# Optimization experiments

Measured on AMD Instinct MI355X. Metric: run time of the kernel, lower is better.

## Reference

```python
import jax, jax.numpy as jnp
import numpy as np
from jax import lax

EPS = 1e-5

def _layernorm(x, g, b):
    m = x.mean(-1, keepdims=True)
    v = ((x - m) ** 2).mean(-1, keepdims=True)
    return (x - m) * lax.rsqrt(v + EPS) * g + b

def _batchnorm(x, g, b):
    # x: [N, C, L]; training-mode batch statistics (torch BatchNorm1d default)
    m = x.mean((0, 2), keepdims=True)
    v = ((x - m) ** 2).mean((0, 2), keepdims=True)
    return (x - m) * lax.rsqrt(v + EPS) * g[None, :, None] + b[None, :, None]

def _conv1d(x, w, bias, stride):
    y = lax.conv_general_dilated(x, w, window_strides=(stride,), padding='VALID',
                                 dimension_numbers=('NCH', 'OIH', 'NCH'))
    return y + bias[None, :, None]

def setup_inputs() -> dict:
    key = jax.random.key(0)
    ks = jax.random.split(key, 22)
    B, C, L = 512, 12, 5000
    NF, HID, LAT = 32, 64, 32
    def w(k, shape, fan_in):
        return jax.random.normal(k, shape, jnp.float32) * (1.0 / np.sqrt(fan_in))
    return {
        'x': jax.random.normal(ks[0], (B, C, L), jnp.float32),
        'c1w': w(ks[1], (32, C, 50), C * 50), 'c1b': jnp.zeros((32,), jnp.float32),
        'bn1g': jnp.ones((32,), jnp.float32), 'bn1b': jnp.zeros((32,), jnp.float32),
        'c2w': w(ks[2], (NF, 32, 25), 32 * 25), 'c2b': jnp.zeros((NF,), jnp.float32),
        'bn2g': jnp.ones((NF,), jnp.float32), 'bn2b': jnp.zeros((NF,), jnp.float32),
        'Wi': w(ks[3], (LAT, NF), NF) * 0.5, 'bi': jnp.zeros((LAT,), jnp.float32),
        'ln1g': jnp.ones((LAT,), jnp.float32), 'ln1b': jnp.zeros((LAT,), jnp.float32),
        'Wh': w(ks[4], (HID, LAT), LAT) * 0.5, 'bh': jnp.zeros((HID,), jnp.float32),
        'ln2g': jnp.ones((HID,), jnp.float32), 'ln2b': jnp.zeros((HID,), jnp.float32),
        'Wr': w(ks[5], (LAT, HID), HID) * 0.5, 'br': jnp.zeros((LAT,), jnp.float32),
        'Wo': w(ks[6], (LAT, LAT), LAT), 'bo': jnp.zeros((LAT,), jnp.float32),
    }

def reference(x, c1w, c1b, bn1g, bn1b, c2w, c2b, bn2g, bn2b,
              Wi, bi, ln1g, ln1b, Wh, bh, ln2g, ln2b, Wr, br, Wo, bo):
    # CNN front-end: [B,12,5000] -> [B,32,496] -> [B,32,95]
    h = jax.nn.relu(_batchnorm(_conv1d(x, c1w, c1b, 10), bn1g, bn1b))
    h = jax.nn.relu(_batchnorm(_conv1d(h, c2w, c2b, 5), bn2g, bn2b))
    feats = h.transpose(2, 0, 1)  # [T, B, NF]
    # input_proj + ln1 have no dependence on the recurrent state -> hoist out of loop
    xt_all = _layernorm(jnp.einsum('tbf,lf->tbl', feats, Wi) + bi, ln1g, ln1b)  # [T,B,LAT]

    def step(hstate, xt):
        combined = xt + hstate
        hp = jax.nn.relu(combined @ Wh.T + bh)      # [B, HID]
        hp = _layernorm(hp, ln2g, ln2b)
        hnew = jnp.tanh(hp @ Wr.T + br)             # [B, LAT]
        return hnew, hnew

    h0 = jnp.zeros((x.shape[0], Wr.shape[0]), x.dtype)
    _, outs = lax.scan(step, h0, xt_all)            # outs: [T, B, LAT]
    pooled = outs.mean(0)                           # mean over time
    return pooled @ Wo.T + bo                       # [B, LAT]
```

## Files before the change

kernel.cpp:

```cpp
#include <hip/hip_runtime.h>

#define EPS 1e-5f

#define B    512
#define C_IN 12
#define L_IN 5000
#define C1   32
#define L1   496
#define NF   32
#define L2   95
#define LAT  32
#define HID  64
#define T    L2

typedef short s16x8 __attribute__((ext_vector_type(8)));
typedef float f32x16 __attribute__((ext_vector_type(16)));

__device__ __forceinline__ ushort f2bf(float f) {
    uint u = __builtin_bit_cast(uint, f);
    u += 0x7fff + ((u >> 16) & 1);
    return (ushort)(u >> 16);
}
__device__ __forceinline__ float bf2f(ushort h) {
    return __builtin_bit_cast(float, (uint)h << 16);
}
__device__ __forceinline__ uint pk(float f) {
    ushort h = f2bf(f);
    return (uint)h | ((uint)f2bf(f - bf2f(h)) << 16);
}
__device__ __forceinline__ uint4 pack4(float4 d) {
    return make_uint4(pk(d.x), pk(d.y), pk(d.z), pk(d.w));
}

__global__ void k_prep_w(const float* __restrict__ c1w, const float* __restrict__ c2w,
                         ushort* __restrict__ wfrag1, ushort* __restrict__ wfrag2) {
    int i = blockIdx.x * 256 + threadIdx.x;
    if (i < 6144) {
        int lane = i & 63, r = i >> 6;
        int split = r & 1, s = (r >> 1) & 3, c = r >> 3;
        int oc = lane & 31, kbase = s * 16 + (lane >> 5) * 8;
        ushort o8[8];
#pragma unroll
        for (int j = 0; j < 8; ++j) {
            int kk = kbase + j;
            float w = (kk < 50) ? c1w[oc * 600 + c * 50 + kk] : 0.f;
            ushort hb = f2bf(w);
            o8[j] = split ? f2bf(w - bf2f(hb)) : hb;
        }
        ushort4* dst = reinterpret_cast<ushort4*>(wfrag1) + (size_t)i * 2;
        dst[0] = make_ushort4(o8[0], o8[1], o8[2], o8[3]);
        dst[1] = make_ushort4(o8[4], o8[5], o8[6], o8[7]);
    } else if (i < 14336) {
        int j = i - 6144;
        int lane = j & 63, r = j >> 6;
        int split = r & 1, ks = (r >> 1) & 1, c = r >> 2;
        int oc = lane & 31, kbase = ks * 16 + (lane >> 5) * 8;
        ushort o8[8];
#pragma unroll
        for (int jj = 0; jj < 8; ++jj) {
            int kk = kbase + jj;
            float w = (kk < 25) ? c2w[oc * 800 + c * 25 + kk] : 0.f;
            ushort hb = f2bf(w);
            o8[jj] = split ? f2bf(w - bf2f(hb)) : hb;
        }
        ushort4* dst = reinterpret_cast<ushort4*>(wfrag2) + (size_t)j * 2;
        dst[0] = make_ushort4(o8[0], o8[1], o8[2], o8[3]);
        dst[1] = make_ushort4(o8[4], o8[5], o8[6], o8[7]);
    }
}

__device__ __forceinline__ void conv1_compute(const uint (*xs)[1344], const uint4* wf4,
                                              int c0, int abase, int lane,
                                              f32x16& hh, f32x16& hl, f32x16& lh) {
    for (int cc = 0; cc < 6; ++cc) {
        const int c = c0 + cc;
        const uint* xc = xs[c];
        const uint4* wfc = wf4 + (size_t)c * 512 + lane;
#pragma unroll
        for (int s = 0; s < 4; ++s) {
            const int idx = abase + s * 16;
            uint2 p0 = *reinterpret_cast<const uint2*>(&xc[idx]);
            uint2 p1 = *reinterpret_cast<const uint2*>(&xc[idx + 2]);
            uint2 p2 = *reinterpret_cast<const uint2*>(&xc[idx + 4]);
            uint2 p3 = *reinterpret_cast<const uint2*>(&xc[idx + 6]);
            union { s16x8 v; uint u[4]; } ah, al, bh, bl;
            ah.u[0] = __builtin_amdgcn_perm(p0.y, p0.x, 0x05040100u);
            al.u[0] = __builtin_amdgcn_perm(p0.y, p0.x, 0x07060302u);
            ah.u[1] = __builtin_amdgcn_perm(p1.y, p1.x, 0x05040100u);
            al.u[1] = __builtin_amdgcn_perm(p1.y, p1.x, 0x07060302u);
            ah.u[2] = __builtin_amdgcn_perm(p2.y, p2.x, 0x05040100u);
            al.u[2] = __builtin_amdgcn_perm(p2.y, p2.x, 0x07060302u);
            ah.u[3] = __builtin_amdgcn_perm(p3.y, p3.x, 0x05040100u);
            al.u[3] = __builtin_amdgcn_perm(p3.y, p3.x, 0x07060302u);
            uint4 bq = wfc[s * 128];
            uint4 lq = wfc[s * 128 + 64];
            bh.u[0] = bq.x; bh.u[1] = bq.y; bh.u[2] = bq.z; bh.u[3] = bq.w;
            bl.u[0] = lq.x; bl.u[1] = lq.y; bl.u[2] = lq.z; bl.u[3] = lq.w;
            hh = __builtin_amdgcn_mfma_f32_32x32x16_bf16(ah.v, bh.v, hh, 0, 0, 0);
            hl = __builtin_amdgcn_mfma_f32_32x32x16_bf16(ah.v, bl.v, hl, 0, 0, 0);
            lh = __builtin_amdgcn_mfma_f32_32x32x16_bf16(al.v, bh.v, lh, 0, 0, 0);
        }
    }
}

__global__ __launch_bounds__(512, 4) void k_conv1(const float* __restrict__ x,
                                                  const ushort* __restrict__ wfrag,
                                                  const float* __restrict__ c1b,
                                                  float* __restrict__ y1,
                                                  float* __restrict__ raw1) {
    __shared__ uint xs[C_IN][1344];
    __shared__ float redS[4][32], redQ[4][32];
    const int chunk = blockIdx.x, b = blockIdx.y, tid = threadIdx.x;
    const int t0 = chunk * 128;
    const int v4max = min(336, (5000 - 10 * t0) >> 2);
    const float4* xb4 = reinterpret_cast<const float4*>(x + (size_t)b * (C_IN * L_IN) + 10 * t0);

    uint4* xs4 = reinterpret_cast<uint4*>(&xs[0][0]);
#pragma unroll
    for (int r = 0; r < 2; ++r) {
        float4 rg[4];
#pragma unroll
        for (int i = 0; i < 4; ++i) {
            const int v = tid + (r * 4 + i) * 512;
            const int c = v / 336, i4 = v - c * 336;
            rg[i] = make_float4(0, 0, 0, 0);
            if (v < 4032 && i4 < v4max) rg[i] = xb4[c * 1250 + i4];
        }
#pragma unroll
        for (int i = 0; i < 4; ++i) {
            const int v = tid + (r * 4 + i) * 512;
            if (v < 4032) xs4[v] = pack4(rg[i]);
        }
    }
    __syncthreads();

    const int lane = tid & 63, wv = tid >> 6;
    const int g = wv >> 2;
    const int tw = wv & 3;
    const int cl = lane & 31;
    const int kgrp = lane >> 5;
    const int abase = 10 * (tw * 32 + cl) + kgrp * 8;

    f32x16 hh, hl, lh;
#pragma unroll
    for (int i = 0; i < 16; ++i) { hh[i] = 0.f; hl[i] = 0.f; lh[i] = 0.f; }
    const uint4* wf4 = reinterpret_cast<const uint4*>(wfrag);

    conv1_compute(xs, wf4, g * 6, abase, lane, hh, hl, lh);

    f32x16 tot;
#pragma unroll
    for (int i = 0; i < 16; ++i) tot[i] = hh[i] + hl[i] + lh[i];

    __syncthreads();
    float4* pr = reinterpret_cast<float4*>(&xs[0][0]);
    if (g == 1) {
#pragma unroll
        for (int i4 = 0; i4 < 4; ++i4)
            pr[tw * 256 + i4 * 64 + lane] =
                make_float4(tot[4*i4], tot[4*i4+1], tot[4*i4+2], tot[4*i4+3]);
    }
    __syncthreads();

    float sum = 0.f, sq = 0.f;
    if (g == 0) {
        const float bias = c1b[cl];
        float* yb = y1 + ((size_t)b * C1 + cl) * L1;
#pragma unroll
        for (int q = 0; q < 4; ++q) {
            float4 p = pr[tw * 256 + q * 64 + lane];
            const int trow = t0 + tw * 32 + 8 * q + 4 * kgrp;
            float4 st;
            st.x = tot[4*q+0] + p.x + bias;
            st.y = tot[4*q+1] + p.y + bias;
            st.z = tot[4*q+2] + p.z + bias;
            st.w = tot[4*q+3] + p.w + bias;
            if (trow < L1) {
                *reinterpret_cast<float4*>(yb + trow) = st;
                sum += st.x + st.y + st.z + st.w;
                sq  += st.x * st.x + st.y * st.y + st.z * st.z + st.w * st.w;
            }
        }
        sum += __shfl_xor(sum, 32);
        sq  += __shfl_xor(sq, 32);
        if (lane < 32) { redS[tw][cl] = sum; redQ[tw][cl] = sq; }
    }
    __syncthreads();
    if (tid < 64) {
        int o = tid & 31, isQ = tid >> 5;
        float v = isQ ? (redQ[0][o] + redQ[1][o] + redQ[2][o] + redQ[3][o])
                      : (redS[0][o] + redS[1][o] + redS[2][o] + redS[3][o]);
        atomicAdd(&raw1[(isQ ? 1024 : 0) + o * 16], v);
    }
}

__global__ __launch_bounds__(384, 3) void k_conv2(const float* __restrict__ y1,
                                                  const ushort* __restrict__ wfrag2,
                                                  const float* __restrict__ c2b,
                                                  const float* __restrict__ raw1,
                                                  const float* __restrict__ bn1g,
                                                  const float* __restrict__ bn1b,
                                                  float* __restrict__ y2,
                                                  float* __restrict__ raw2) {
    __shared__ uint xs[C1][512];
    __shared__ float fin[64];
    __shared__ float redS[3][32], redQ[3][32];
    const int b = blockIdx.x, tid = threadIdx.x;

    if (tid < 32) {
        const float cnt = 1.f / (float)(B * L1);
        float mean = raw1[tid * 16] * cnt;
        float var = raw1[1024 + tid * 16] * cnt - mean * mean;
        float sc = bn1g[tid] * rsqrtf(var + EPS);
        fin[tid] = sc;
        fin[32 + tid] = bn1b[tid] - mean * sc;
    }
    __syncthreads();

    const float4* src = reinterpret_cast<const float4*>(y1 + (size_t)b * (C1 * L1));
    for (int v = tid; v < C1 * 128; v += 384) {
        const int c = v >> 7, i4 = v & 127;
        uint4 o = make_uint4(0, 0, 0, 0);
        if (i4 < 124) {
            const float sc = fin[c], sh = fin[32 + c];
            float4 d = src[c * 124 + i4];
            float e0 = fmaxf(fmaf(d.x, sc, sh), 0.f);
            float e1 = fmaxf(fmaf(d.y, sc, sh), 0.f);
            float e2 = fmaxf(fmaf(d.z, sc, sh), 0.f);
            float e3 = fmaxf(fmaf(d.w, sc, sh), 0.f);
            o = make_uint4(pk(e0), pk(e1), pk(e2), pk(e3));
        }
        *reinterpret_cast<uint4*>(&xs[c][4 * i4]) = o;
    }
    __syncthreads();

    const int lane = tid & 63, wv = tid >> 6;
    const int g = (wv >= 3) ? 1 : 0;
    const int tw = wv - 3 * g;
    const int cl = lane & 31;
    const int kgrp = lane >> 5;
    const int tbase = 5 * (tw * 32 + cl) + kgrp * 8;

    f32x16 hh, hl, lh;
#pragma unroll
    for (int i = 0; i < 16; ++i) { hh[i] = 0.f; hl[i] = 0.f; lh[i] = 0.f; }
    const uint4* wf4 = reinterpret_cast<const uint4*>(wfrag2);

    for (int cc = 0; cc < 16; ++cc) {
        const int c = g * 16 + cc;
        const uint* xc = xs[c];
        const uint4* wfc = wf4 + (size_t)c * 256 + lane;
#pragma unroll
        for (int ks = 0; ks < 2; ++ks) {
            const int idx = tbase + ks * 16;
            uint u0 = xc[idx + 0], u1 = xc[idx + 1], u2 = xc[idx + 2], u3 = xc[idx + 3];
            uint u4 = xc[idx + 4], u5 = xc[idx + 5], u6 = xc[idx + 6], u7 = xc[idx + 7];
            union { s16x8 v; uint u[4]; } ah, al, bh, bl;
            ah.u[0] = __builtin_amdgcn_perm(u1, u0, 0x05040100u);
            al.u[0] = __builtin_amdgcn_perm(u1, u0, 0x07060302u);
            ah.u[1] = __builtin_amdgcn_perm(u3, u2, 0x05040100u);
            al.u[1] = __builtin_amdgcn_perm(u3, u2, 0x07060302u);
            ah.u[2] = __builtin_amdgcn_perm(u5, u4, 0x05040100u);
            al.u[2] = __builtin_amdgcn_perm(u5, u4, 0x07060302u);
            ah.u[3] = __builtin_amdgcn_perm(u7, u6, 0x05040100u);
            al.u[3] = __builtin_amdgcn_perm(u7, u6, 0x07060302u);
            uint4 bq = wfc[ks * 128];
            uint4 lq = wfc[ks * 128 + 64];
            bh.u[0] = bq.x; bh.u[1] = bq.y; bh.u[2] = bq.z; bh.u[3] = bq.w;
            bl.u[0] = lq.x; bl.u[1] = lq.y; bl.u[2] = lq.z; bl.u[3] = lq.w;
            hh = __builtin_amdgcn_mfma_f32_32x32x16_bf16(ah.v, bh.v, hh, 0, 0, 0);
            hl = __builtin_amdgcn_mfma_f32_32x32x16_bf16(ah.v, bl.v, hl, 0, 0, 0);
            lh = __builtin_amdgcn_mfma_f32_32x32x16_bf16(al.v, bh.v, lh, 0, 0, 0);
        }
    }

    f32x16 tot;
#pragma unroll
    for (int i = 0; i < 16; ++i) tot[i] = hh[i] + hl[i] + lh[i];

    __syncthreads();
    float4* pr = reinterpret_cast<float4*>(&xs[0][0]);
    if (g == 1) {
#pragma unroll
        for (int i4 = 0; i4 < 4; ++i4)
            pr[tw * 256 + i4 * 64 + lane] =
                make_float4(tot[4*i4], tot[4*i4+1], tot[4*i4+2], tot[4*i4+3]);
    }
    __syncthreads();

    float sum = 0.f, sq = 0.f;
    if (g == 0) {
        const float bias = c2b[cl];
#pragma unroll
        for (int q = 0; q < 4; ++q) {
            float4 p = pr[tw * 256 + q * 64 + lane];
            float v4[4] = { tot[4*q+0] + p.x + bias, tot[4*q+1] + p.y + bias,
                            tot[4*q+2] + p.z + bias, tot[4*q+3] + p.w + bias };
#pragma unroll
            for (int j = 0; j < 4; ++j) {
                const int t = tw * 32 + 8 * q + 4 * kgrp + j;
                if (t < L2) {
                    y2[((size_t)b * L2 + t) * NF + cl] = v4[j];
                    sum += v4[j]; sq += v4[j] * v4[j];
                }
            }
        }
        sum += __shfl_xor(sum, 32);
        sq  += __shfl_xor(sq, 32);
        if (lane < 32) { redS[tw][cl] = sum; redQ[tw][cl] = sq; }
    }
    __syncthreads();
    if (tid < 64) {
        int o = tid & 31, isQ = tid >> 5;
        float v = isQ ? (redQ[0][o] + redQ[1][o] + redQ[2][o])
                      : (redS[0][o] + redS[1][o] + redS[2][o]);
        atomicAdd(&raw2[(isQ ? 1024 : 0) + o * 16], v);
    }
}

__global__ __launch_bounds__(256) void k_proj(const float* __restrict__ y2,
                                              const float* __restrict__ raw2,
                                              const float* __restrict__ bn2g,
                                              const float* __restrict__ bn2b,
                                              const float* __restrict__ Wi,
                                              const float* __restrict__ bi,
                                              const float* __restrict__ ln1g,
                                              const float* __restrict__ ln1b,
                                              const float* __restrict__ Wh,
                                              const float* __restrict__ bh,
                                              float* __restrict__ xt2) {
    __shared__ float fin[64];
    if (threadIdx.x < 32) {
        const float cnt = 1.f / (float)(B * L2);
        float mean = raw2[threadIdx.x * 16] * cnt;
        float var = raw2[1024 + threadIdx.x * 16] * cnt - mean * mean;
        float sc = bn2g[threadIdx.x] * rsqrtf(var + EPS);
        fin[threadIdx.x] = sc;
        fin[32 + threadIdx.x] = bn2b[threadIdx.x] - mean * sc;
    }
    __syncthreads();

    const int r = blockIdx.x * 256 + threadIdx.x;
    const int b = r / 95, t = r - b * 95;

    const float4* row = reinterpret_cast<const float4*>(y2 + (size_t)r * NF);
    float u[NF];
#pragma unroll
    for (int f4 = 0; f4 < 8; ++f4) {
        float4 v = row[f4];
        u[4*f4]   = fmaxf(fmaf(v.x, fin[4*f4],   fin[32 + 4*f4]),   0.f);
        u[4*f4+1] = fmaxf(fmaf(v.y, fin[4*f4+1], fin[32 + 4*f4+1]), 0.f);
        u[4*f4+2] = fmaxf(fmaf(v.z, fin[4*f4+2], fin[32 + 4*f4+2]), 0.f);
        u[4*f4+3] = fmaxf(fmaf(v.w, fin[4*f4+3], fin[32 + 4*f4+3]), 0.f);
    }
    float xln[LAT];
    float s = 0.f, q = 0.f;
#pragma unroll
    for (int l = 0; l < LAT; ++l) {
        float a = bi[l];
#pragma unroll
        for (int f = 0; f < NF; ++f) a = fmaf(u[f], Wi[l * NF + f], a);
        xln[l] = a; s += a; q += a * a;
    }
    const float m = s * (1.f / LAT);
    const float inv = rsqrtf(q * (1.f / LAT) - m * m + EPS);
#pragma unroll
    for (int l = 0; l < LAT; ++l) xln[l] = (xln[l] - m) * inv * ln1g[l] + ln1b[l];

    float4* dst = reinterpret_cast<float4*>(xt2 + ((size_t)t * B + b) * HID);
#pragma unroll
    for (int j4 = 0; j4 < 16; ++j4) {
        float4 o4;
        float a0 = bh[4*j4], a1 = bh[4*j4+1], a2 = bh[4*j4+2], a3 = bh[4*j4+3];
#pragma unroll
        for (int l = 0; l < LAT; ++l) {
            float xl = xln[l];
            a0 = fmaf(xl, Wh[(4*j4)   * LAT + l], a0);
            a1 = fmaf(xl, Wh[(4*j4+1) * LAT + l], a1);
            a2 = fmaf(xl, Wh[(4*j4+2) * LAT + l], a2);
            a3 = fmaf(xl, Wh[(4*j4+3) * LAT + l], a3);
        }
        o4.x = a0; o4.y = a1; o4.z = a2; o4.w = a3;
        dst[j4] = o4;
    }
}

__global__ __launch_bounds__(64) void k_rnn(const float* __restrict__ xt2,
                                            const float* __restrict__ Wh,
                                            const float* __restrict__ ln2g,
                                            const float* __restrict__ ln2b,
                                            const float* __restrict__ Wr,
                                            const float* __restrict__ br,
                                            const float* __restrict__ Wo,
                                            const float* __restrict__ bo,
                                            float* __restrict__ out) {
    __shared__ __align__(16) float aS[64];
    __shared__ __align__(16) float hS[32];
    const int lane = threadIdx.x;
    const int b = blockIdx.x;
    const int l = lane & 31;

    float whv[LAT];
#pragma unroll
    for (int i = 0; i < LAT; ++i) whv[i] = Wh[lane * LAT + i];

    float wg[HID];
    float S1 = 0.f, S2 = br[l];
#pragma unroll
    for (int j = 0; j < HID; ++j) {
        float w = Wr[l * HID + j];
        wg[j] = w * ln2g[j];
        S1 += wg[j];
        S2 = fmaf(w, ln2b[j], S2);
    }

    float hfull[LAT];
#pragma unroll
    for (int i = 0; i < LAT; ++i) hfull[i] = 0.f;
    float pooled = 0.f;
    float xq = xt2[(size_t)b * HID + lane];

    for (int t = 0; t < T; ++t) {
        float xq_next = 0.f;
        if (t + 1 < T) xq_next = xt2[((size_t)(t + 1) * B + b) * HID + lane];

        float a0 = xq, a1 = 0.f, a2c = 0.f, a3c = 0.f;
#pragma unroll
        for (int i = 0; i < 8; ++i) {
            a0  = fmaf(hfull[4*i+0], whv[4*i+0], a0);
            a1  = fmaf(hfull[4*i+1], whv[4*i+1], a1);
            a2c = fmaf(hfull[4*i+2], whv[4*i+2], a2c);
            a3c = fmaf(hfull[4*i+3], whv[4*i+3], a3c);
        }
        const float a = fmaxf((a0 + a1) + (a2c + a3c), 0.f);

        aS[lane] = a;
        asm volatile("s_waitcnt lgkmcnt(0)" ::: "memory");

        float d0 = 0.f, d1 = 0.f, d2 = 0.f, d3 = 0.f;
#pragma unroll
        for (int i = 0; i < 16; ++i) {
            float4 v = reinterpret_cast<const float4*>(aS)[i];
            d0 = fmaf(v.x, wg[4*i+0], d0); d1 = fmaf(v.y, wg[4*i+1], d1);
            d2 = fmaf(v.z, wg[4*i+2], d2); d3 = fmaf(v.w, wg[4*i+3], d3);
        }
        float s = a, q = a * a;
#pragma unroll
        for (int off = 32; off >= 1; off >>= 1) { s += __shfl_xor(s, off); q += __shfl_xor(q, off); }
        const float m = s * (1.f / HID);
        const float inv = __builtin_amdgcn_rsqf(q * (1.f / HID) - m * m + EPS);
        const float dot = (d0 + d1) + (d2 + d3);
        const float a2v = fmaf(inv, dot - m * S1, S2);

        const float z = __builtin_amdgcn_exp2f(2.8853900817779268f * a2v);
        const float h = 1.f - 2.f * __builtin_amdgcn_rcpf(z + 1.f);
        pooled += h;

        if (lane < 32) hS[lane] = h;
        asm volatile("s_waitcnt lgkmcnt(0)" ::: "memory");
#pragma unroll
        for (int i = 0; i < 8; ++i) {
            float4 hv = reinterpret_cast<const float4*>(hS)[i];
            hfull[4*i] = hv.x; hfull[4*i+1] = hv.y; hfull[4*i+2] = hv.z; hfull[4*i+3] = hv.w;
        }
        xq = xq_next;
    }
    pooled *= (1.f / T);
    if (lane < 32) aS[lane] = pooled;
    asm volatile("s_waitcnt lgkmcnt(0)" ::: "memory");

    float wov[LAT];
#pragma unroll
    for (int i = 0; i < LAT; ++i) wov[i] = Wo[l * LAT + i];
    float b0 = bo[l], b1 = 0.f, b2 = 0.f, b3 = 0.f;
#pragma unroll
    for (int i = 0; i < 8; ++i) {
        float4 pv = reinterpret_cast<const float4*>(aS)[i];
        b0 = fmaf(pv.x, wov[4*i+0], b0); b1 = fmaf(pv.y, wov[4*i+1], b1);
        b2 = fmaf(pv.z, wov[4*i+2], b2); b3 = fmaf(pv.w, wov[4*i+3], b3);
    }
    if (lane < 32) out[(size_t)b * LAT + l] = (b0 + b1) + (b2 + b3);
}

extern "C" void kernel_launch(void* const* d_in, const int* in_sizes, int n_in,
                              void* d_out, int out_size, void* d_ws, size_t ws_size,
                              hipStream_t stream) {
    const float* x    = (const float*)d_in[0];
    const float* c1w  = (const float*)d_in[1];
    const float* c1b  = (const float*)d_in[2];
    const float* bn1g = (const float*)d_in[3];
    const float* bn1b = (const float*)d_in[4];
    const float* c2w  = (const float*)d_in[5];
    const float* c2b  = (const float*)d_in[6];
    const float* bn2g = (const float*)d_in[7];
    const float* bn2b = (const float*)d_in[8];
    const float* Wi   = (const float*)d_in[9];
    const float* bi   = (const float*)d_in[10];
    const float* ln1g = (const float*)d_in[11];
    const float* ln1b = (const float*)d_in[12];
    const float* Wh   = (const float*)d_in[13];
    const float* bh   = (const float*)d_in[14];
    const float* ln2g = (const float*)d_in[15];
    const float* ln2b = (const float*)d_in[16];
    const float* Wr   = (const float*)d_in[17];
    const float* br   = (const float*)d_in[18];
    const float* Wo   = (const float*)d_in[19];
    const float* bo   = (const float*)d_in[20];

    float* ws = (float*)d_ws;
    float* raw1 = ws;
    float* raw2 = ws + 2048;
    ushort* wfrag1 = (ushort*)(ws + 4096);
    ushort* wfrag2 = (ushort*)(ws + 28672);
    float* y1   = ws + 61440;
    float* y2   = ws + 8187904;
    float* xt2  = y1;
    float* out  = (float*)d_out;

    hipMemsetAsync(raw1, 0, 4096 * sizeof(float), stream);
    k_prep_w<<<56, 256, 0, stream>>>(c1w, c2w, wfrag1, wfrag2);
    k_conv1<<<dim3(4, B), 512, 0, stream>>>(x, wfrag1, c1b, y1, raw1);
    k_conv2<<<B, 384, 0, stream>>>(y1, wfrag2, c2b, raw1, bn1g, bn1b, y2, raw2);
    k_proj<<<190, 256, 0, stream>>>(y2, raw2, bn2g, bn2b, Wi, bi, ln1g, ln1b, Wh, bh, xt2);
    k_rnn<<<B, 64, 0, stream>>>(xt2, Wh, ln2g, ln2b, Wr, br, Wo, bo, out);
}
```

Before: 228.8 us.

## Halve conv1 time tile and split channels across four wave groups

k_conv1 now processes 64 output timesteps per block instead of 128, launching 8 chunks per batch row, and splits the 12 input channels across 4 wave groups of 3 channels instead of 2 groups of 6. Partial MFMA accumulators from three groups are reduced through shared memory by group 0. This shrinks shared memory per block and shortens the serial MFMA chain per wave to raise parallelism and occupancy, at the cost of more cross-wave reduction traffic and more blocks and atomics. k_conv2 changes are only cosmetic indexing.

```diff
diff --git a/kernel.cpp b/kernel.cpp
--- a/kernel.cpp
+++ b/kernel.cpp
@@ -69,12 +69,54 @@
     }
 }
 
-__device__ __forceinline__ void conv1_compute(const uint (*xs)[1344], const uint4* wf4,
-                                              int c0, int abase, int lane,
-                                              f32x16& hh, f32x16& hl, f32x16& lh) {
-    for (int cc = 0; cc < 6; ++cc) {
-        const int c = c0 + cc;
-        const uint* xc = xs[c];
+__global__ __launch_bounds__(512, 4) void k_conv1(const float* __restrict__ x,
+                                                  const ushort* __restrict__ wfrag,
+                                                  const float* __restrict__ c1b,
+                                                  float* __restrict__ y1,
+                                                  float* __restrict__ raw1) {
+    __shared__ uint xs[C_IN * 704];
+    __shared__ float redS[2][32], redQ[2][32];
+    const int chunk = blockIdx.x, b = blockIdx.y, tid = threadIdx.x;
+    const int t0 = chunk * 64;
+    const int fbase = chunk * 640;
+    const int v4max = min(176, (L_IN - fbase) >> 2);
+    const float4* xb4 = reinterpret_cast<const float4*>(x + (size_t)b * (C_IN * L_IN) + fbase);
+
+    float4 rg[5];
+#pragma unroll
+    for (int r = 0; r < 5; ++r) {
+        const int v = tid + r * 512;
+        rg[r] = make_float4(0, 0, 0, 0);
+        if (v < 2112) {
+            const int c = v / 176, i4 = v - c * 176;
+            if (i4 < v4max) rg[r] = xb4[c * 1250 + i4];
+        }
+    }
+#pragma unroll
+    for (int r = 0; r < 5; ++r) {
+        const int v = tid + r * 512;
+        if (v < 2112) {
+            const int c = v / 176, i4 = v - c * 176;
+            *reinterpret_cast<uint4*>(&xs[c * 704 + 4 * i4]) = pack4(rg[r]);
+        }
+    }
+    __syncthreads();
+
+    const int lane = tid & 63, wv = tid >> 6;
+    const int tw = wv & 1;
+    const int g = wv >> 1;
+    const int cl = lane & 31;
+    const int kgrp = lane >> 5;
+    const int abase = 10 * (tw * 32 + cl) + kgrp * 8;
+
+    f32x16 hh, hl, lh;
+#pragma unroll
+    for (int i = 0; i < 16; ++i) { hh[i] = 0.f; hl[i] = 0.f; lh[i] = 0.f; }
+    const uint4* wf4 = reinterpret_cast<const uint4*>(wfrag);
+
+    for (int cc = 0; cc < 3; ++cc) {
+        const int c = g * 3 + cc;
+        const uint* xc = xs + c * 704;
         const uint4* wfc = wf4 + (size_t)c * 512 + lane;
 #pragma unroll
         for (int s = 0; s < 4; ++s) {
@@ -101,80 +143,44 @@
             lh = __builtin_amdgcn_mfma_f32_32x32x16_bf16(al.v, bh.v, lh, 0, 0, 0);
         }
     }
-}
-
-__global__ __launch_bounds__(512, 4) void k_conv1(const float* __restrict__ x,
-                                                  const ushort* __restrict__ wfrag,
-                                                  const float* __restrict__ c1b,
-                                                  float* __restrict__ y1,
-                                                  float* __restrict__ raw1) {
-    __shared__ uint xs[C_IN][1344];
-    __shared__ float redS[4][32], redQ[4][32];
-    const int chunk = blockIdx.x, b = blockIdx.y, tid = threadIdx.x;
-    const int t0 = chunk * 128;
-    const int v4max = min(336, (5000 - 10 * t0) >> 2);
-    const float4* xb4 = reinterpret_cast<const float4*>(x + (size_t)b * (C_IN * L_IN) + 10 * t0);
-
-    uint4* xs4 = reinterpret_cast<uint4*>(&xs[0][0]);
-#pragma unroll
-    for (int r = 0; r < 2; ++r) {
-        float4 rg[4];
-#pragma unroll
-        for (int i = 0; i < 4; ++i) {
-            const int v = tid + (r * 4 + i) * 512;
-            const int c = v / 336, i4 = v - c * 336;
-            rg[i] = make_float4(0, 0, 0, 0);
-            if (v < 4032 && i4 < v4max) rg[i] = xb4[c * 1250 + i4];
-        }
-#pragma unroll
-        for (int i = 0; i < 4; ++i) {
-            const int v = tid + (r * 4 + i) * 512;
-            if (v < 4032) xs4[v] = pack4(rg[i]);
-        }
-    }
-    __syncthreads();
-
-    const int lane = tid & 63, wv = tid >> 6;
-    const int g = wv >> 2;
-    const int tw = wv & 3;
-    const int cl = lane & 31;
-    const int kgrp = lane >> 5;
-    const int abase = 10 * (tw * 32 + cl) + kgrp * 8;
-
-    f32x16 hh, hl, lh;
-#pragma unroll
-    for (int i = 0; i < 16; ++i) { hh[i] = 0.f; hl[i] = 0.f; lh[i] = 0.f; }
-    const uint4* wf4 = reinterpret_cast<const uint4*>(wfrag);
-
-    conv1_compute(xs, wf4, g * 6, abase, lane, hh, hl, lh);
 
     f32x16 tot;
 #pragma unroll
     for (int i = 0; i < 16; ++i) tot[i] = hh[i] + hl[i] + lh[i];
 
     __syncthreads();
-    float4* pr = reinterpret_cast<float4*>(&xs[0][0]);
-    if (g == 1) {
-#pragma unroll
-        for (int i4 = 0; i4 < 4; ++i4)
-            pr[tw * 256 + i4 * 64 + lane] =
-                make_float4(tot[4*i4], tot[4*i4+1], tot[4*i4+2], tot[4*i4+3]);
-    }
-    __syncthreads();
-
-    float sum = 0.f, sq = 0.f;
+    float4* pr = reinterpret_cast<float4*>(xs);
+    if (g != 0) {
+        const int slot = ((g - 1) * 2 + tw) * 256;
+#pragma unroll
+        for (int q = 0; q < 4; ++q)
+            pr[slot + q * 64 + lane] =
+                make_float4(tot[4*q], tot[4*q+1], tot[4*q+2], tot[4*q+3]);
+    }
+    __syncthreads();
+
     if (g == 0) {
+#pragma unroll
+        for (int pg = 0; pg < 3; ++pg) {
+            const int slot = (pg * 2 + tw) * 256;
+#pragma unroll
+            for (int q = 0; q < 4; ++q) {
+                float4 p = pr[slot + q * 64 + lane];
+                tot[4*q+0] += p.x; tot[4*q+1] += p.y;
+                tot[4*q+2] += p.z; tot[4*q+3] += p.w;
+            }
+        }
         const float bias = c1b[cl];
+        float sum = 0.f, sq = 0.f;
         float* yb = y1 + ((size_t)b * C1 + cl) * L1;
 #pragma unroll
         for (int q = 0; q < 4; ++q) {
-            float4 p = pr[tw * 256 + q * 64 + lane];
             const int trow = t0 + tw * 32 + 8 * q + 4 * kgrp;
             float4 st;
-            st.x = tot[4*q+0] + p.x + bias;
-            st.y = tot[4*q+1] + p.y + bias;
-            st.z = tot[4*q+2] + p.z + bias;
-            st.w = tot[4*q+3] + p.w + bias;
+            st.x = tot[4*q+0] + bias;
+            st.y = tot[4*q+1] + bias;
+            st.z = tot[4*q+2] + bias;
+            st.w = tot[4*q+3] + bias;
             if (trow < L1) {
                 *reinterpret_cast<float4*>(yb + trow) = st;
                 sum += st.x + st.y + st.z + st.w;
@@ -188,8 +194,8 @@
     __syncthreads();
     if (tid < 64) {
         int o = tid & 31, isQ = tid >> 5;
-        float v = isQ ? (redQ[0][o] + redQ[1][o] + redQ[2][o] + redQ[3][o])
-                      : (redS[0][o] + redS[1][o] + redS[2][o] + redS[3][o]);
+        float v = isQ ? (redQ[0][o] + redQ[1][o])
+                      : (redS[0][o] + redS[1][o]);
         atomicAdd(&raw1[(isQ ? 1024 : 0) + o * 16], v);
     }
 }
@@ -202,7 +208,7 @@
                                                   const float* __restrict__ bn1b,
                                                   float* __restrict__ y2,
                                                   float* __restrict__ raw2) {
-    __shared__ uint xs[C1][512];
+    __shared__ uint xs[C1 * 512];
     __shared__ float fin[64];
     __shared__ float redS[3][32], redQ[3][32];
     const int b = blockIdx.x, tid = threadIdx.x;
@@ -230,11 +236,11 @@
             float e3 = fmaxf(fmaf(d.w, sc, sh), 0.f);
             o = make_uint4(pk(e0), pk(e1), pk(e2), pk(e3));
         }
-        *reinterpret_cast<uint4*>(&xs[c][4 * i4]) = o;
-    }
-    __syncthreads();
-
-    const int lane = tid & 63, wv = tid >> 6;
+        *reinterpret_cast<uint4*>(&xs[c * 512 + 4 * i4]) = o;
+    }
+    __syncthreads();
+
+    const int lane = tid & 63, wv = tid / 64;
     const int g = (wv >= 3) ? 1 : 0;
     const int tw = wv - 3 * g;
     const int cl = lane & 31;
@@ -248,7 +254,7 @@
 
     for (int cc = 0; cc < 16; ++cc) {
         const int c = g * 16 + cc;
-        const uint* xc = xs[c];
+        const uint* xc = xs + c * 512;
         const uint4* wfc = wf4 + (size_t)c * 256 + lane;
 #pragma unroll
         for (int ks = 0; ks < 2; ++ks) {
@@ -279,12 +285,12 @@
     for (int i = 0; i < 16; ++i) tot[i] = hh[i] + hl[i] + lh[i];
 
     __syncthreads();
-    float4* pr = reinterpret_cast<float4*>(&xs[0][0]);
+    float4* pr = reinterpret_cast<float4*>(xs);
     if (g == 1) {
 #pragma unroll
-        for (int i4 = 0; i4 < 4; ++i4)
-            pr[tw * 256 + i4 * 64 + lane] =
-                make_float4(tot[4*i4], tot[4*i4+1], tot[4*i4+2], tot[4*i4+3]);
+        for (int q = 0; q < 4; ++q)
+            pr[tw * 256 + q * 64 + lane] =
+                make_float4(tot[4*q], tot[4*q+1], tot[4*q+2], tot[4*q+3]);
     }
     __syncthreads();
 
@@ -519,7 +525,7 @@
 
     hipMemsetAsync(raw1, 0, 4096 * sizeof(float), stream);
     k_prep_w<<<56, 256, 0, stream>>>(c1w, c2w, wfrag1, wfrag2);
-    k_conv1<<<dim3(4, B), 512, 0, stream>>>(x, wfrag1, c1b, y1, raw1);
+    k_conv1<<<dim3(8, B), 512, 0, stream>>>(x, wfrag1, c1b, y1, raw1);
     k_conv2<<<B, 384, 0, stream>>>(y1, wfrag2, c2b, raw1, bn1g, bn1b, y2, raw2);
     k_proj<<<190, 256, 0, stream>>>(y2, raw2, bn2g, bn2b, Wi, bi, ln1g, ln1b, Wh, bh, xt2);
     k_rnn<<<B, 64, 0, stream>>>(xt2, Wh, ln2g, ln2b, Wr, br, Wo, bo, out);
```

Result: slower. 271.8 us (+18.8%).
